# Kernel tuning notes

Hardware: AMD Instinct MI355X
Metric: run time of the kernel (lower is better)

Reference implementation:

```python
import jax, jax.numpy as jnp
import numpy as np

EPS = 1e-09
TOP_K = 2


def setup_inputs() -> dict:
    key = jax.random.key(0)
    k1, k2 = jax.random.split(key)
    N, D, E = 32768, 1024, 64
    x = jax.random.normal(k1, (N, D), dtype=jnp.float32)
    gate_w = jax.random.normal(k2, (E, D), dtype=jnp.float32) * (1.0 / np.sqrt(D))
    return {"x": x, "gate_w": gate_w}


def reference(x, gate_w):
    # logits: [N, E] = x @ gate_w.T  (nn.Linear with no bias)
    logits = jnp.einsum("nd,ed->ne", x, gate_w)
    probs = jax.nn.softmax(logits, axis=-1)
    # aux load-balancing loss (stored on buffer in torch; returned here)
    mean_probs = probs.mean(axis=0)  # [E]
    aux_loss = jnp.sum(mean_probs * jnp.log(mean_probs + EPS))
    # top-k selection + renormalize
    top_k_weights, top_k_indices = jax.lax.top_k(probs, TOP_K)  # [N, K]
    top_k_weights = top_k_weights / (top_k_weights.sum(axis=-1, keepdims=True) + EPS)
    return top_k_weights, top_k_indices, aux_loss
```

## Files before the change

kernel.cpp:

```cpp
#include <hip/hip_runtime.h>
#include <hip/hip_bf16.h>
#include <math.h>

#define NROWS 32768
#define DDIM  1024
#define NEXP  64
#define TAU   2e-4f
#define EPSF  1e-9f
#define CAPMAX 8192
#define NSHARD 8
#define NCH   32

typedef __attribute__((ext_vector_type(8)))  short  short8;
typedef __attribute__((ext_vector_type(16))) float  f32x16;
typedef __attribute__((address_space(3))) unsigned int       lds_u32;
typedef __attribute__((address_space(1))) const unsigned int g_u32;

__device__ __forceinline__ bool gt_(float a, int ea, float b, int eb)
{ return a > b || (a == b && ea < eb); }

__device__ __forceinline__ void cvt_hl(float f, short& h, short& l)
{
    __hip_bfloat16 hb = __float2bfloat16(f);
    float r = f - __bfloat162float(hb);
    __hip_bfloat16 lb = __float2bfloat16(r);
    h = *reinterpret_cast<short*>(&hb);
    l = *reinterpret_cast<short*>(&lb);
}

__global__ void wpack_kernel(const float* __restrict__ gw,
                             unsigned short* __restrict__ wp,
                             float* __restrict__ shard,
                             int* __restrict__ cnt)
{
    if (blockIdx.x == 0) {
        shard[threadIdx.x]       = 0.0f;
        shard[256 + threadIdx.x] = 0.0f;
        if (threadIdx.x == 0) *cnt = 0;
    }
    const int kc = blockIdx.x;
    const int t  = threadIdx.x;
    const int lane = t & 63, g = (t >> 6) & 1, pr = t >> 7;
    const int e = g * 32 + (lane & 31);
    const int k = kc * 16 + (lane >> 5) * 8;
    float4 f0 = *reinterpret_cast<const float4*>(gw + (size_t)e * DDIM + k);
    float4 f1 = *reinterpret_cast<const float4*>(gw + (size_t)e * DDIM + k + 4);
    float f[8] = {f0.x, f0.y, f0.z, f0.w, f1.x, f1.y, f1.z, f1.w};
    short8 o;
    #pragma unroll
    for (int j = 0; j < 8; ++j) {
        short hh, ll;
        cvt_hl(f[j], hh, ll);
        o[j] = pr ? ll : hh;
    }
    *reinterpret_cast<short8*>(wp + ((size_t)((kc * 2 + g) * 2 + pr) * 64 + lane) * 8) = o;
}

__global__ __launch_bounds__(256, 4) void moe_main(
    const float* __restrict__ x, const unsigned short* __restrict__ wp,
    float* __restrict__ out, float* __restrict__ shard,
    int* __restrict__ cnt, int* __restrict__ list, int cap)
{
    extern __shared__ char smem[];

    const int t = threadIdx.x;
    const int wave = t >> 6, lane = t & 63;
    const int wm = wave & 1, g = wave >> 1;
    const int l31 = lane & 31, l5 = lane >> 5;
    const int row0 = blockIdx.x * 64;
    const int arow = wm * 32 + l31;
    const int xr   = (arow & 7) << 4;

    f32x16 acc;
    #pragma unroll
    for (int r = 0; r < 16; ++r) acc[r] = 0.0f;

    int srow[2], scol[2];
    #pragma unroll
    for (int q = 0; q < 2; ++q) {
        int d = q * 4096 + t * 16;
        srow[q] = d >> 7;
        scol[q] = (d & 127) ^ ((srow[q] & 7) << 4);
    }

    const char* wqb = (const char*)wp + (size_t)g * 2048 + (size_t)lane * 16;

    #define STAGE(c_) do {                                                       \
        const char* xs0_ = (const char*)x + (size_t)row0 * 4096 + (size_t)(c_) * 128; \
        const int xb_ = ((c_) & 3) * 8192;                                       \
        _Pragma("unroll")                                                        \
        for (int q_ = 0; q_ < 2; ++q_) {                                         \
            int d_ = q_ * 4096 + t * 16;                                         \
            const char* xsrc_ = xs0_ + (size_t)srow[q_] * 4096 + scol[q_];       \
            __builtin_amdgcn_global_load_lds((g_u32*)xsrc_,                      \
                (lds_u32*)(smem + xb_ + d_), 16, 0, 0);                          \
        }                                                                        \
    } while (0)

    #define BLOAD(dst0, dst1, dst2, dst3, c_) do {                               \
        const char* b_ = wqb + (size_t)(c_) * 8192;                              \
        dst0 = *reinterpret_cast<const short8*>(b_);                             \
        dst1 = *reinterpret_cast<const short8*>(b_ + 1024);                      \
        dst2 = *reinterpret_cast<const short8*>(b_ + 4096);                      \
        dst3 = *reinterpret_cast<const short8*>(b_ + 5120);                      \
    } while (0)

    short8 Bc0, Bc1, Bc2, Bc3, Bn0, Bn1, Bn2, Bn3;

    STAGE(0); STAGE(1); STAGE(2);
    BLOAD(Bc0, Bc1, Bc2, Bc3, 0);

    for (int i = 0; i < NCH; ++i) {
        if (i < NCH - 1) BLOAD(Bn0, Bn1, Bn2, Bn3, i + 1);
        if (i < NCH - 3) STAGE(i + 3);
        __builtin_amdgcn_sched_barrier(0);
        if (i == 0)               { asm volatile("s_waitcnt vmcnt(6)" ::: "memory"); }
        else if (i < NCH - 3)     { asm volatile("s_waitcnt vmcnt(8)" ::: "memory"); }
        else if (i == NCH - 3)    { asm volatile("s_waitcnt vmcnt(6)" ::: "memory"); }
        else if (i == NCH - 2)    { asm volatile("s_waitcnt vmcnt(4)" ::: "memory"); }
        else                      { asm volatile("s_waitcnt vmcnt(0)" ::: "memory"); }
        __builtin_amdgcn_s_barrier();
        __builtin_amdgcn_sched_barrier(0);

        const int xb = (i & 3) * 8192;
        #pragma unroll
        for (int kcl = 0; kcl < 2; ++kcl) {
            const int cb = kcl * 64 + l5 * 32;
            const char* xrow = smem + xb + arow * 128;
            float4 f0 = *reinterpret_cast<const float4*>(xrow + (cb ^ xr));
            float4 f1 = *reinterpret_cast<const float4*>(xrow + ((cb + 16) ^ xr));
            float f[8] = {f0.x, f0.y, f0.z, f0.w, f1.x, f1.y, f1.z, f1.w};
            short8 ah, al;
            #pragma unroll
            for (int jj = 0; jj < 8; ++jj) {
                short hh, ll;
                cvt_hl(f[jj], hh, ll);
                ah[jj] = hh; al[jj] = ll;
            }
            short8 bh = kcl ? Bc2 : Bc0;
            short8 bl = kcl ? Bc3 : Bc1;
            acc = __builtin_amdgcn_mfma_f32_32x32x16_bf16(ah, bh, acc, 0, 0, 0);
            acc = __builtin_amdgcn_mfma_f32_32x32x16_bf16(al, bh, acc, 0, 0, 0);
            acc = __builtin_amdgcn_mfma_f32_32x32x16_bf16(ah, bl, acc, 0, 0, 0);
        }
        Bc0 = Bn0; Bc1 = Bn1; Bc2 = Bn2; Bc3 = Bn3;
        __builtin_amdgcn_sched_barrier(0);
        __builtin_amdgcn_s_barrier();
        __builtin_amdgcn_sched_barrier(0);
    }
    #undef STAGE
    #undef BLOAD

    float* lgs = reinterpret_cast<float*>(smem);
    __syncthreads();
    #pragma unroll
    for (int r = 0; r < 16; ++r) {
        const int lrow = wm * 32 + (r & 3) + 8 * (r >> 2) + 4 * l5;
        lgs[lrow * 68 + g * 32 + l31] = acc[r];
    }
    __syncthreads();

    const int erow = t >> 2, q = t & 3;
    float L[16];
    #pragma unroll
    for (int i = 0; i < 4; ++i) {
        float4 v = *reinterpret_cast<const float4*>(lgs + erow * 68 + q * 16 + i * 4);
        L[4*i] = v.x; L[4*i+1] = v.y; L[4*i+2] = v.z; L[4*i+3] = v.w;
    }
    float v1 = -3.4e38f, v2 = -3.4e38f, v3 = -3.4e38f;
    int   e1 = 1 << 30,  e2 = 1 << 30,  e3 = 1 << 30;
    #pragma unroll
    for (int i = 0; i < 16; ++i) {
        float v = L[i]; int e = q * 16 + i;
        if      (gt_(v, e, v1, e1)) { v3=v2; e3=e2; v2=v1; e2=e1; v1=v; e1=e; }
        else if (gt_(v, e, v2, e2)) { v3=v2; e3=e2; v2=v; e2=e; }
        else if (gt_(v, e, v3, e3)) { v3=v; e3=e; }
    }
    #pragma unroll
    for (int m = 1; m <= 2; m <<= 1) {
        float o1 = __shfl_xor(v1, m), o2 = __shfl_xor(v2, m), o3 = __shfl_xor(v3, m);
        int  oe1 = __shfl_xor(e1, m), oe2 = __shfl_xor(e2, m), oe3 = __shfl_xor(e3, m);
        float n1, n2, n3; int m1, m2, m3;
        if (gt_(v1, e1, o1, oe1)) {
            n1 = v1; m1 = e1;
            if (gt_(v2, e2, o1, oe1)) {
                n2 = v2; m2 = e2;
                if (gt_(v3, e3, o1, oe1)) { n3 = v3; m3 = e3; } else { n3 = o1; m3 = oe1; }
            } else {
                n2 = o1; m2 = oe1;
                if (gt_(v2, e2, o2, oe2)) { n3 = v2; m3 = e2; } else { n3 = o2; m3 = oe2; }
            }
        } else {
            n1 = o1; m1 = oe1;
            if (gt_(o2, oe2, v1, e1)) {
                n2 = o2; m2 = oe2;
                if (gt_(o3, oe3, v1, e1)) { n3 = o3; m3 = oe3; } else { n3 = v1; m3 = e1; }
            } else {
                n2 = v1; m2 = e1;
                if (gt_(o2, oe2, v2, e2)) { n3 = o2; m3 = oe2; } else { n3 = v2; m3 = e2; }
            }
        }
        v1 = n1; e1 = m1; v2 = n2; e2 = m2; v3 = n3; e3 = m3;
    }
    float pr[16], sl = 0.0f;
    #pragma unroll
    for (int i = 0; i < 16; ++i) { pr[i] = expf(L[i] - v1); sl += pr[i]; }
    float S = sl;
    S += __shfl_xor(S, 1); S += __shfl_xor(S, 2);
    const float invS = 1.0f / S;
    #pragma unroll
    for (int i = 0; i < 16; ++i) pr[i] *= invS;
    #pragma unroll
    for (int m = 4; m <= 32; m <<= 1)
        #pragma unroll
        for (int i = 0; i < 16; ++i) pr[i] += __shfl_xor(pr[i], m);
    float* auxred = lgs + 64 * 68;
    if (lane < 4) {
        #pragma unroll
        for (int i = 0; i < 16; ++i) auxred[wave * 64 + q * 16 + i] = pr[i];
    }
    if (q == 0) {
        const float p1 = invS;
        const float p2 = expf(v2 - v1) * invS;
        const float dn = p1 + p2 + EPSF;
        const int r = row0 + erow;
        out[2 * r]                 = p1 / dn;
        out[2 * r + 1]             = p2 / dn;
        out[2 * NROWS + 2 * r]     = (float)e1;
        out[2 * NROWS + 2 * r + 1] = (float)e2;
        if (cap > 0 && (v1 - v2 < TAU || v2 - v3 < TAU)) {
            int pos = atomicAdd(cnt, 1);
            if (pos < cap) list[pos] = r;
        }
    }
    __syncthreads();
    if (t < 64) {
        float s = auxred[t] + auxred[64 + t] + auxred[128 + t] + auxred[192 + t];
        atomicAdd(&shard[(blockIdx.x & (NSHARD - 1)) * 64 + t], s);
    }
}

__global__ __launch_bounds__(256) void finalize_kernel(
    const float* __restrict__ x, const float* __restrict__ gw,
    float* __restrict__ out, const float* __restrict__ shard,
    const int* __restrict__ cnt, const int* __restrict__ list, int cap)
{
    if (blockIdx.x == 0) {
        const int tt = threadIdx.x;
        if (tt < 64) {
            float m = 0.0f;
            #pragma unroll
            for (int s = 0; s < NSHARD; ++s) m += shard[s * 64 + tt];
            m *= (1.0f / (float)NROWS);
            float v = m * logf(m + EPSF);
            #pragma unroll
            for (int k = 1; k <= 32; k <<= 1) v += __shfl_xor(v, k);
            if (tt == 0) out[4 * NROWS] = v;
        }
        return;
    }
    __shared__ float lg[64];
    const int n = (cap > 0) ? min(*cnt, cap) : 0;
    const int tt = threadIdx.x, e = tt >> 2, part = tt & 3;
    for (int j = (int)blockIdx.x - 1; j < n; j += 64) {
        const int row = list[j];
        const float* xrp = x  + (size_t)row * DDIM + part * 256;
        const float* wrp = gw + (size_t)e   * DDIM + part * 256;
        float a = 0.0f;
        #pragma unroll 8
        for (int kk = 0; kk < 64; ++kk) {
            float4 xv = *reinterpret_cast<const float4*>(xrp + kk * 4);
            float4 wv = *reinterpret_cast<const float4*>(wrp + kk * 4);
            a += xv.x * wv.x + xv.y * wv.y + xv.z * wv.z + xv.w * wv.w;
        }
        a += __shfl_xor(a, 1); a += __shfl_xor(a, 2);
        if (part == 0) lg[e] = a;
        __syncthreads();
        if (tt < 4) {
            const int q = tt;
            float v1 = -3.4e38f, v2 = -3.4e38f; int e1 = 1 << 30, e2 = 1 << 30;
            float Lr[16];
            #pragma unroll
            for (int i = 0; i < 16; ++i) {
                float v = Lr[i] = lg[q * 16 + i]; int ee = q * 16 + i;
                if      (gt_(v, ee, v1, e1)) { v2 = v1; e2 = e1; v1 = v; e1 = ee; }
                else if (gt_(v, ee, v2, e2)) { v2 = v; e2 = ee; }
            }
            #pragma unroll
            for (int m = 1; m <= 2; m <<= 1) {
                float o1 = __shfl_xor(v1, m), o2 = __shfl_xor(v2, m);
                int  oe1 = __shfl_xor(e1, m), oe2 = __shfl_xor(e2, m);
                float n1, n2; int m1, m2;
                if (gt_(v1, e1, o1, oe1)) {
                    n1 = v1; m1 = e1;
                    if (gt_(v2, e2, o1, oe1)) { n2 = v2; m2 = e2; } else { n2 = o1; m2 = oe1; }
                } else {
                    n1 = o1; m1 = oe1;
                    if (gt_(o2, oe2, v1, e1)) { n2 = o2; m2 = oe2; } else { n2 = v1; m2 = e1; }
                }
                v1 = n1; e1 = m1; v2 = n2; e2 = m2;
            }
            float s = 0.0f;
            #pragma unroll
            for (int i = 0; i < 16; ++i) s += expf(Lr[i] - v1);
            s += __shfl_xor(s, 1); s += __shfl_xor(s, 2);
            if (q == 0) {
                const float invS = 1.0f / s;
                const float p1 = invS, p2 = expf(v2 - v1) * invS;
                const float dn = p1 + p2 + EPSF;
                out[2 * row]                 = p1 / dn;
                out[2 * row + 1]             = p2 / dn;
                out[2 * NROWS + 2 * row]     = (float)e1;
                out[2 * NROWS + 2 * row + 1] = (float)e2;
            }
        }
        __syncthreads();
    }
}

extern "C" void kernel_launch(void* const* d_in, const int* in_sizes, int n_in,
                              void* d_out, int out_size, void* d_ws, size_t ws_size,
                              hipStream_t stream)
{
    const float* x  = (const float*)d_in[0];
    const float* gw = (const float*)d_in[1];
    float* out      = (float*)d_out;

    unsigned short* wp = (unsigned short*)d_ws;
    float* shard   = (float*)((char*)d_ws + 262144);
    int*   cnt     = (int*)((char*)d_ws + 264192);
    int*   list    = (int*)((char*)d_ws + 264448);
    int cap = 0;
    if (ws_size >= 264448 + 4096) {
        size_t avail = (ws_size - 264448) / sizeof(int);
        cap = (avail > CAPMAX) ? CAPMAX : (int)avail;
    }

    hipLaunchKernelGGL(wpack_kernel, dim3(64), dim3(256), 0, stream,
                       gw, wp, shard, cnt);
    hipLaunchKernelGGL(moe_main, dim3(NROWS / 64), dim3(256), 32768, stream,
                       x, wp, out, shard, cnt, list, cap);
    hipLaunchKernelGGL(finalize_kernel, dim3(65), dim3(256), 0, stream,
                       x, gw, out, shard, cnt, list, cap);
}
```

Measured before the change: 61.65 us.

## Shrink row tile to 32 rows with 2 waves and double the K chunk per stage

The main GEMM kernel now uses 32-row blocks of 128 threads (2 waves, each covering 32 experts) instead of 64-row blocks of 256 threads. Each pipeline stage now stages 64 floats of K per row instead of 32, so there are half as many loop iterations and barriers. The vmcnt waits and the bf16 weight register prefetch are rescaled to match. The aim is more blocks and fewer sync points per block, at the cost of twice the weight reads from L2 and fewer waves per block to hide latency.

```diff
diff --git a/kernel.cpp b/kernel.cpp
--- a/kernel.cpp
+++ b/kernel.cpp
@@ -9,7 +9,7 @@
 #define EPSF  1e-9f
 #define CAPMAX 8192
 #define NSHARD 8
-#define NCH   32
+#define NCH   16
 
 typedef __attribute__((ext_vector_type(8)))  short  short8;
 typedef __attribute__((ext_vector_type(16))) float  f32x16;
@@ -56,7 +56,7 @@
     *reinterpret_cast<short8*>(wp + ((size_t)((kc * 2 + g) * 2 + pr) * 64 + lane) * 8) = o;
 }
 
-__global__ __launch_bounds__(256, 4) void moe_main(
+__global__ __launch_bounds__(128, 2) void moe_main(
     const float* __restrict__ x, const unsigned short* __restrict__ wp,
     float* __restrict__ out, float* __restrict__ shard,
     int* __restrict__ cnt, int* __restrict__ list, int cap)
@@ -64,69 +64,70 @@
     extern __shared__ char smem[];
 
     const int t = threadIdx.x;
-    const int wave = t >> 6, lane = t & 63;
-    const int wm = wave & 1, g = wave >> 1;
+    const int g = t >> 6;
+    const int lane = t & 63;
     const int l31 = lane & 31, l5 = lane >> 5;
-    const int row0 = blockIdx.x * 64;
-    const int arow = wm * 32 + l31;
+    const int row0 = blockIdx.x * 32;
+    const int arow = l31;
     const int xr   = (arow & 7) << 4;
 
     f32x16 acc;
     #pragma unroll
     for (int r = 0; r < 16; ++r) acc[r] = 0.0f;
 
-    int srow[2], scol[2];
-    #pragma unroll
-    for (int q = 0; q < 2; ++q) {
-        int d = q * 4096 + t * 16;
-        srow[q] = d >> 7;
-        scol[q] = (d & 127) ^ ((srow[q] & 7) << 4);
+    int srow[4], scol[4];
+    #pragma unroll
+    for (int q = 0; q < 4; ++q) {
+        int d = q * 2048 + t * 16;
+        srow[q] = d >> 8;
+        scol[q] = (d & 255) ^ ((srow[q] & 7) << 4);
     }
 
     const char* wqb = (const char*)wp + (size_t)g * 2048 + (size_t)lane * 16;
 
     #define STAGE(c_) do {                                                       \
-        const char* xs0_ = (const char*)x + (size_t)row0 * 4096 + (size_t)(c_) * 128; \
+        const char* xs0_ = (const char*)x + (size_t)row0 * 4096 + (size_t)(c_) * 256; \
         const int xb_ = ((c_) & 3) * 8192;                                       \
         _Pragma("unroll")                                                        \
-        for (int q_ = 0; q_ < 2; ++q_) {                                         \
-            int d_ = q_ * 4096 + t * 16;                                         \
+        for (int q_ = 0; q_ < 4; ++q_) {                                         \
+            int d_ = q_ * 2048 + t * 16;                                         \
             const char* xsrc_ = xs0_ + (size_t)srow[q_] * 4096 + scol[q_];       \
             __builtin_amdgcn_global_load_lds((g_u32*)xsrc_,                      \
                 (lds_u32*)(smem + xb_ + d_), 16, 0, 0);                          \
         }                                                                        \
     } while (0)
 
-    #define BLOAD(dst0, dst1, dst2, dst3, c_) do {                               \
-        const char* b_ = wqb + (size_t)(c_) * 8192;                              \
-        dst0 = *reinterpret_cast<const short8*>(b_);                             \
-        dst1 = *reinterpret_cast<const short8*>(b_ + 1024);                      \
-        dst2 = *reinterpret_cast<const short8*>(b_ + 4096);                      \
-        dst3 = *reinterpret_cast<const short8*>(b_ + 5120);                      \
+    #define BLOAD(dst_, c_) do {                                                 \
+        _Pragma("unroll")                                                        \
+        for (int kcl_ = 0; kcl_ < 4; ++kcl_) {                                   \
+            const char* b_ = wqb + (size_t)((c_) * 4 + kcl_) * 4096;             \
+            dst_[kcl_][0] = *reinterpret_cast<const short8*>(b_);                \
+            dst_[kcl_][1] = *reinterpret_cast<const short8*>(b_ + 1024);         \
+        }                                                                        \
     } while (0)
 
-    short8 Bc0, Bc1, Bc2, Bc3, Bn0, Bn1, Bn2, Bn3;
+    short8 Bc[4][2], Bn[4][2];
 
     STAGE(0); STAGE(1); STAGE(2);
-    BLOAD(Bc0, Bc1, Bc2, Bc3, 0);
+    BLOAD(Bc, 0);
 
     for (int i = 0; i < NCH; ++i) {
-        if (i < NCH - 1) BLOAD(Bn0, Bn1, Bn2, Bn3, i + 1);
+        if (i < NCH - 1) BLOAD(Bn, i + 1);
         if (i < NCH - 3) STAGE(i + 3);
         __builtin_amdgcn_sched_barrier(0);
-        if (i == 0)               { asm volatile("s_waitcnt vmcnt(6)" ::: "memory"); }
-        else if (i < NCH - 3)     { asm volatile("s_waitcnt vmcnt(8)" ::: "memory"); }
-        else if (i == NCH - 3)    { asm volatile("s_waitcnt vmcnt(6)" ::: "memory"); }
-        else if (i == NCH - 2)    { asm volatile("s_waitcnt vmcnt(4)" ::: "memory"); }
+        if (i == 0)               { asm volatile("s_waitcnt vmcnt(12)" ::: "memory"); }
+        else if (i < NCH - 3)     { asm volatile("s_waitcnt vmcnt(16)" ::: "memory"); }
+        else if (i == NCH - 3)    { asm volatile("s_waitcnt vmcnt(12)" ::: "memory"); }
+        else if (i == NCH - 2)    { asm volatile("s_waitcnt vmcnt(8)" ::: "memory"); }
         else                      { asm volatile("s_waitcnt vmcnt(0)" ::: "memory"); }
         __builtin_amdgcn_s_barrier();
         __builtin_amdgcn_sched_barrier(0);
 
         const int xb = (i & 3) * 8192;
+        const char* xrow = smem + xb + arow * 256;
         #pragma unroll
-        for (int kcl = 0; kcl < 2; ++kcl) {
+        for (int kcl = 0; kcl < 4; ++kcl) {
             const int cb = kcl * 64 + l5 * 32;
-            const char* xrow = smem + xb + arow * 128;
             float4 f0 = *reinterpret_cast<const float4*>(xrow + (cb ^ xr));
             float4 f1 = *reinterpret_cast<const float4*>(xrow + ((cb + 16) ^ xr));
             float f[8] = {f0.x, f0.y, f0.z, f0.w, f1.x, f1.y, f1.z, f1.w};
@@ -137,13 +138,15 @@
                 cvt_hl(f[jj], hh, ll);
                 ah[jj] = hh; al[jj] = ll;
             }
-            short8 bh = kcl ? Bc2 : Bc0;
-            short8 bl = kcl ? Bc3 : Bc1;
-            acc = __builtin_amdgcn_mfma_f32_32x32x16_bf16(ah, bh, acc, 0, 0, 0);
-            acc = __builtin_amdgcn_mfma_f32_32x32x16_bf16(al, bh, acc, 0, 0, 0);
-            acc = __builtin_amdgcn_mfma_f32_32x32x16_bf16(ah, bl, acc, 0, 0, 0);
-        }
-        Bc0 = Bn0; Bc1 = Bn1; Bc2 = Bn2; Bc3 = Bn3;
+            acc = __builtin_amdgcn_mfma_f32_32x32x16_bf16(ah, Bc[kcl][0], acc, 0, 0, 0);
+            acc = __builtin_amdgcn_mfma_f32_32x32x16_bf16(al, Bc[kcl][0], acc, 0, 0, 0);
+            acc = __builtin_amdgcn_mfma_f32_32x32x16_bf16(ah, Bc[kcl][1], acc, 0, 0, 0);
+        }
+        #pragma unroll
+        for (int kcl = 0; kcl < 4; ++kcl) {
+            Bc[kcl][0] = Bn[kcl][0];
+            Bc[kcl][1] = Bn[kcl][1];
+        }
         __builtin_amdgcn_sched_barrier(0);
         __builtin_amdgcn_s_barrier();
         __builtin_amdgcn_sched_barrier(0);
@@ -155,7 +158,7 @@
     __syncthreads();
     #pragma unroll
     for (int r = 0; r < 16; ++r) {
-        const int lrow = wm * 32 + (r & 3) + 8 * (r >> 2) + 4 * l5;
+        const int lrow = (r & 3) + 8 * (r >> 2) + 4 * l5;
         lgs[lrow * 68 + g * 32 + l31] = acc[r];
     }
     __syncthreads();
@@ -214,10 +217,10 @@
     for (int m = 4; m <= 32; m <<= 1)
         #pragma unroll
         for (int i = 0; i < 16; ++i) pr[i] += __shfl_xor(pr[i], m);
-    float* auxred = lgs + 64 * 68;
+    float* auxred = lgs + 32 * 68;
     if (lane < 4) {
         #pragma unroll
-        for (int i = 0; i < 16; ++i) auxred[wave * 64 + q * 16 + i] = pr[i];
+        for (int i = 0; i < 16; ++i) auxred[g * 64 + q * 16 + i] = pr[i];
     }
     if (q == 0) {
         const float p1 = invS;
@@ -235,7 +238,7 @@
     }
     __syncthreads();
     if (t < 64) {
-        float s = auxred[t] + auxred[64 + t] + auxred[128 + t] + auxred[192 + t];
+        float s = auxred[t] + auxred[64 + t];
         atomicAdd(&shard[(blockIdx.x & (NSHARD - 1)) * 64 + t], s);
     }
 }
@@ -338,7 +341,7 @@
 
     hipLaunchKernelGGL(wpack_kernel, dim3(64), dim3(256), 0, stream,
                        gw, wp, shard, cnt);
-    hipLaunchKernelGGL(moe_main, dim3(NROWS / 64), dim3(256), 32768, stream,
+    hipLaunchKernelGGL(moe_main, dim3(NROWS / 32), dim3(128), 32768, stream,
                        x, wp, out, shard, cnt, list, cap);
     hipLaunchKernelGGL(finalize_kernel, dim3(65), dim3(256), 0, stream,
                        x, gw, out, shard, cnt, list, cap);
```

Result: no change. 61.36 us (-0.5%).
